# Kernel tuning notes

Hardware: AMD Instinct MI355X
Metric: run time of the kernel (lower is better)

Reference implementation:

```python
import jax, jax.numpy as jnp
import numpy as np

HIDDEN = 1024
JOINTS = 21
IN_DIM = JOINTS * 3  # 63
BATCH = 64
SEQ = 512


def setup_inputs() -> dict:
    key = jax.random.key(0)
    ks = jax.random.split(key, 11)
    s = 0.02
    f32 = jnp.float32
    return {
        "real_seq": jax.random.normal(ks[0], (BATCH, SEQ, IN_DIM), f32),
        # PyTorch nn.GRU params (gates ordered r, z, n)
        "W_ih": jax.random.normal(ks[1], (3 * HIDDEN, IN_DIM), f32) * s,
        "W_hh": jax.random.normal(ks[2], (3 * HIDDEN, HIDDEN), f32) * s,
        "b_ih": jax.random.normal(ks[3], (3 * HIDDEN,), f32) * s,
        "b_hh": jax.random.normal(ks[4], (3 * HIDDEN,), f32) * s,
        # projector MLP (no nonlinearities in the original)
        "W1": jax.random.normal(ks[5], (HIDDEN, HIDDEN), f32) * s,
        "b1": jax.random.normal(ks[6], (HIDDEN,), f32) * s,
        "W2": jax.random.normal(ks[7], (HIDDEN, HIDDEN), f32) * s,
        "b2": jax.random.normal(ks[8], (HIDDEN,), f32) * s,
        "W3": jax.random.normal(ks[9], (IN_DIM, HIDDEN), f32) * s,
        "b3": jax.random.normal(ks[10], (IN_DIM,), f32) * s,
        "condition_length": 5,
        "ground_truth_length": 5,
    }


def _condition_list(seq_len, condition_length, ground_truth_length):
    gt = np.ones((100, ground_truth_length))
    co = np.zeros((100, condition_length))
    return np.concatenate((gt, co), 1).reshape(-1)[:seq_len]


def reference(real_seq, W_ih, W_hh, b_ih, b_hh, W1, b1, W2, b2, W3, b3,
              condition_length, ground_truth_length):
    B, T, D = real_seq.shape
    H = W_hh.shape[1]
    cond = jnp.asarray(_condition_list(T, condition_length, ground_truth_length),
                       dtype=real_seq.dtype)  # [T], static 1/0 teacher-forcing pattern

    h0 = jnp.zeros((B, H), real_seq.dtype)
    o0 = jnp.zeros((B, D), real_seq.dtype)
    xs = (jnp.transpose(real_seq, (1, 0, 2)), cond)  # time-major

    def step(carry, x):
        h, out = carry
        xt, c = x
        inp = jnp.where(c > 0.5, xt, out)  # teacher-forcing switch
        gi = inp @ W_ih.T + b_ih           # [B, 3H]
        gh = h @ W_hh.T + b_hh             # [B, 3H]
        i_r, i_z, i_n = jnp.split(gi, 3, axis=-1)
        h_r, h_z, h_n = jnp.split(gh, 3, axis=-1)
        r = jax.nn.sigmoid(i_r + h_r)
        z = jax.nn.sigmoid(i_z + h_z)
        n = jnp.tanh(i_n + r * h_n)
        h_new = (1.0 - z) * n + z * h
        lin = (h_new @ W1.T + b1) @ W2.T + b2
        out_new = inp + lin @ W3.T + b3    # residual velocities
        return (h_new, out_new), out_new

    _, outs = jax.lax.scan(step, (h0, o0), xs)  # outs: [T, B, D]
    return jnp.transpose(outs, (1, 0, 2)).reshape(B, T, D // 3, 3)
```

## Files before the change

kernel.cpp:

```cpp
#include <hip/hip_runtime.h>
#include <hip/hip_bf16.h>


#define HIDDEN 1024
#define INDIM  63
#define TSEQ   512
#define MB     16
#define NGRP   4
#define NBLK   64
#define HWORDS 512

typedef __attribute__((ext_vector_type(8))) short bfrag8;
typedef __attribute__((ext_vector_type(4))) float ffrag4;
typedef unsigned long long ull;

#define MFMA_B16(a, b, c) __builtin_amdgcn_mfma_f32_16x16x32_bf16((a), (b), (c), 0, 0, 0)

__device__ __forceinline__ short f2bf(float x) {
  __hip_bfloat16 b = __float2bfloat16(x);
  return __builtin_bit_cast(short, b);
}
__device__ __forceinline__ float bf2f(short s) {
  unsigned u = ((unsigned)(unsigned short)s) << 16;
  return __builtin_bit_cast(float, u);
}


__global__ void k_t1(const float* __restrict__ W2, const float* __restrict__ b1,
                     const float* __restrict__ b2, float* __restrict__ t1) {
  const int w = threadIdx.x >> 6, lane = threadIdx.x & 63;
  const int o = blockIdx.x * 4 + w;
  if (o >= HIDDEN) return;
  const float* row = W2 + (size_t)o * HIDDEN;
  float s = 0.f;
  for (int k = lane; k < HIDDEN; k += 64) s += row[k] * b1[k];
  for (int off = 32; off; off >>= 1) s += __shfl_down(s, off, 64);
  if (lane == 0) t1[o] = s + b2[o];
}

__global__ void k_bp(const float* __restrict__ W3, const float* __restrict__ t1,
                     const float* __restrict__ b3, float* __restrict__ bp) {
  const int w = threadIdx.x >> 6, lane = threadIdx.x & 63;
  for (int d = w; d < INDIM; d += 4) {
    const float* row = W3 + (size_t)d * HIDDEN;
    float s = 0.f;
    for (int k = lane; k < HIDDEN; k += 64) s += row[k] * t1[k];
    for (int off = 32; off; off >>= 1) s += __shfl_down(s, off, 64);
    if (lane == 0) bp[d] = s + b3[d];
  }
}

__global__ void k_gemm(const float* __restrict__ A, const float* __restrict__ B,
                       float* __restrict__ C, int M, int N, int K) {
  __shared__ float As[16][17], Bs[16][17];
  const int tx = threadIdx.x, ty = threadIdx.y;
  const int row = blockIdx.y * 16 + ty;
  const int col = blockIdx.x * 16 + tx;
  float acc = 0.f;
  for (int k0 = 0; k0 < K; k0 += 16) {
    As[ty][tx] = (row < M) ? A[(size_t)row * K + k0 + tx] : 0.f;
    Bs[ty][tx] = B[(size_t)(k0 + ty) * N + col];
    __syncthreads();
#pragma unroll
    for (int kk = 0; kk < 16; ++kk) acc += As[ty][kk] * Bs[kk][tx];
    __syncthreads();
  }
  if (row < M && col < N) C[(size_t)row * N + col] = acc;
}


__global__ __launch_bounds__(256, 1) void k_main(
    const float* __restrict__ X,
    const float* __restrict__ W_ih, const float* __restrict__ W_hh,
    const float* __restrict__ b_ih, const float* __restrict__ b_hh,
    const float* __restrict__ WpF, const float* __restrict__ bpF,
    const int* __restrict__ pCL, const int* __restrict__ pGT,
    ull* __restrict__ hb, float* __restrict__ OUT) {
  __shared__ short h_st[MB][HIDDEN + 8];
  __shared__ short inp_bf[MB][88];
  __shared__ float inp_f[MB][68];
  __shared__ float gt_z[MB][16], gt_hn[MB][16];
  __shared__ float gt_ir[MB][16], gt_iz[MB][16], gt_in[MB][16];
  __shared__ short htmp[MB][16];

  const int tid = threadIdx.x;
  const int w = tid >> 6;
  const int lane = tid & 63;
  const int c = lane & 15;
  const int quad = lane >> 4;
  const int g = blockIdx.x >> 6;
  const int j = blockIdx.x & 63;

  const int gtv = pGT[0];
  int period = pCL[0] + gtv;
  if (period < 1) period = 1;

  bfrag8 wB[32];
  bfrag8 wp[32];
  if (w < 3) {
    const float* wr = W_hh + ((size_t)w * HIDDEN + (size_t)j * 16 + c) * HIDDEN;
#pragma unroll
    for (int ks = 0; ks < 32; ++ks) {
      const float* p = wr + ks * 32 + quad * 8;
      bfrag8 f;
#pragma unroll
      for (int e = 0; e < 8; ++e) f[e] = f2bf(p[e]);
      wB[ks] = f;
    }
  } else {
#pragma unroll
    for (int gate = 0; gate < 3; ++gate) {
      const float* wr = W_ih + ((size_t)gate * HIDDEN + (size_t)j * 16 + c) * INDIM;
#pragma unroll
      for (int ks = 0; ks < 2; ++ks) {
        bfrag8 f;
#pragma unroll
        for (int e = 0; e < 8; ++e) {
          int k = ks * 32 + quad * 8 + e;
          f[e] = (k < INDIM) ? f2bf(wr[k]) : (short)0;
        }
        wB[gate * 2 + ks] = f;
      }
    }
  }
  const int dd = 16 * w + c;
  {
    const float* wr = WpF + (size_t)dd * HIDDEN;
#pragma unroll
    for (int ks = 0; ks < 32; ++ks) {
      bfrag8 f;
#pragma unroll
      for (int e = 0; e < 8; ++e)
        f[e] = (dd < INDIM) ? f2bf(wr[ks * 32 + quad * 8 + e]) : (short)0;
      wp[ks] = f;
    }
  }

  float bias_g;
  if (w == 0)      bias_g = b_ih[j * 16 + c] + b_hh[j * 16 + c];
  else if (w == 1) bias_g = b_ih[HIDDEN + j * 16 + c] + b_hh[HIDDEN + j * 16 + c];
  else if (w == 2) bias_g = b_hh[2 * HIDDEN + j * 16 + c];
  else             bias_g = b_ih[2 * HIDDEN + j * 16 + c];
  const float bp_l = (dd < INDIM) ? bpF[dd] : 0.f;

  for (int i = tid; i < MB * (HIDDEN + 8); i += 256) ((short*)h_st)[i] = 0;
  for (int i = tid; i < MB * 88; i += 256) ((short*)inp_bf)[i] = 0;
  for (int i = tid; i < MB * 68; i += 256) ((float*)inp_f)[i] = 0.f;

  ull* hb_g[2] = {hb + (size_t)g * MB * HWORDS,
                  hb + (size_t)(NGRP + g) * MB * HWORDS};

  for (int t = 0; t < TSEQ; ++t) {
    const unsigned tg = (unsigned)(t + 1);
    const bool teach = ((t % period) < gtv);
    if (teach) {
      const int row = tid >> 4, d0 = (tid & 15) * 4;
      const float* xr = X + ((size_t)(g * MB + row) * TSEQ + t) * INDIM;
#pragma unroll
      for (int e = 0; e < 4; ++e) {
        int d = d0 + e;
        float v = (d < INDIM) ? xr[d] : 0.f;
        inp_f[row][d] = v;
        inp_bf[row][d] = f2bf(v);
      }
    }
    __syncthreads();

    ffrag4 ghr;
    float hp[4];
    if (w < 3) {
      ffrag4 acc[4];
#pragma unroll
      for (int e = 0; e < 4; ++e) {
        acc[0][e] = bias_g; acc[1][e] = 0.f; acc[2][e] = 0.f; acc[3][e] = 0.f;
      }
#pragma unroll
      for (int ks = 0; ks < 32; ++ks) {
        const bfrag8 a = *(const bfrag8*)&h_st[c][ks * 32 + quad * 8];
        acc[ks & 3] = MFMA_B16(a, wB[ks], acc[ks & 3]);
      }
      ffrag4 gsum = acc[0] + acc[1] + acc[2] + acc[3];
      if (w == 1) {
#pragma unroll
        for (int i = 0; i < 4; ++i) gt_z[quad * 4 + i][c] = gsum[i];
      } else if (w == 2) {
#pragma unroll
        for (int i = 0; i < 4; ++i) gt_hn[quad * 4 + i][c] = gsum[i];
      } else {
        ghr = gsum;
#pragma unroll
        for (int i = 0; i < 4; ++i) hp[i] = bf2f(h_st[quad * 4 + i][j * 16 + c]);
      }
    } else {
      ffrag4 gir, giz, gin;
#pragma unroll
      for (int e = 0; e < 4; ++e) { gir[e] = 0.f; giz[e] = 0.f; gin[e] = bias_g; }
#pragma unroll
      for (int ks = 0; ks < 2; ++ks) {
        const bfrag8 a = *(const bfrag8*)&inp_bf[c][ks * 32 + quad * 8];
        gir = MFMA_B16(a, wB[0 + ks], gir);
        giz = MFMA_B16(a, wB[2 + ks], giz);
        gin = MFMA_B16(a, wB[4 + ks], gin);
      }
#pragma unroll
      for (int i = 0; i < 4; ++i) {
        gt_ir[quad * 4 + i][c] = gir[i];
        gt_iz[quad * 4 + i][c] = giz[i];
        gt_in[quad * 4 + i][c] = gin[i];
      }
    }
    __syncthreads();

    ull* hw = hb_g[t & 1];
    if (w == 0) {
#pragma unroll
      for (int i = 0; i < 4; ++i) {
        const int row = quad * 4 + i;
        float r = 1.f / (1.f + __expf(-(ghr[i] + gt_ir[row][c])));
        float z = 1.f / (1.f + __expf(-(gt_z[row][c] + gt_iz[row][c])));
        float n = tanhf(gt_in[row][c] + r * gt_hn[row][c]);
        htmp[row][c] = f2bf((1.f - z) * n + z * hp[i]);
      }
      asm volatile("" ::: "memory");
      const int r = lane >> 2, q4 = (lane & 3) * 4;
      unsigned lo0 = (unsigned)(unsigned short)htmp[r][q4 + 0] |
                     ((unsigned)(unsigned short)htmp[r][q4 + 1] << 16);
      unsigned lo1 = (unsigned)(unsigned short)htmp[r][q4 + 2] |
                     ((unsigned)(unsigned short)htmp[r][q4 + 3] << 16);
      ull w0v = ((ull)tg << 32) | lo0;
      ull w1v = ((ull)tg << 32) | lo1;
      ull* dst = hw + (size_t)r * HWORDS + 8 * j + (lane & 3) * 2;
      __hip_atomic_store(dst, w0v, __ATOMIC_RELAXED, __HIP_MEMORY_SCOPE_SYSTEM);
      __hip_atomic_store(dst + 1, w1v, __ATOMIC_RELAXED, __HIP_MEMORY_SCOPE_SYSTEM);
    }

    {
      ull v[32];
#pragma unroll
      for (int s = 0; s < 32; ++s)
        v[s] = __hip_atomic_load(&hw[tid + s * 256], __ATOMIC_RELAXED,
                                 __HIP_MEMORY_SCOPE_SYSTEM);
      bool bad = true;
      while (bad) {
        bad = false;
#pragma unroll
        for (int s = 0; s < 32; ++s) {
          if ((unsigned)(v[s] >> 32) != tg) {
            v[s] = __hip_atomic_load(&hw[tid + s * 256], __ATOMIC_RELAXED,
                                     __HIP_MEMORY_SCOPE_SYSTEM);
            bad = true;
          }
        }
      }
#pragma unroll
      for (int s = 0; s < 32; ++s) {
        const int widx = tid + s * 256;
        *(unsigned*)&h_st[widx >> 9][(widx & 511) * 2] = (unsigned)v[s];
      }
    }
    __syncthreads();

    const bool rep = (t + 1 < TSEQ) && !(((t + 1) % period) < gtv);
    if (rep || j == 0) {
      ffrag4 oa0, oa1;
#pragma unroll
      for (int e = 0; e < 4; ++e) { oa0[e] = bp_l; oa1[e] = 0.f; }
#pragma unroll
      for (int ks = 0; ks < 32; ++ks) {
        const bfrag8 a = *(const bfrag8*)&h_st[c][ks * 32 + quad * 8];
        if (ks & 1) oa1 = MFMA_B16(a, wp[ks], oa1);
        else        oa0 = MFMA_B16(a, wp[ks], oa0);
      }
      ffrag4 o = oa0 + oa1;
#pragma unroll
      for (int i = 0; i < 4; ++i) {
        const int row = quad * 4 + i;
        if (dd < INDIM) {
          float val = o[i] + inp_f[row][dd];
          if (j == 0) OUT[((size_t)(g * MB + row) * TSEQ + t) * INDIM + dd] = val;
          if (rep) { inp_f[row][dd] = val; inp_bf[row][dd] = f2bf(val); }
        } else if (rep) {
          inp_bf[row][dd] = 0;
        }
      }
    }
  }
}


extern "C" void kernel_launch(void* const* d_in, const int* in_sizes, int n_in,
                              void* d_out, int out_size, void* d_ws, size_t ws_size,
                              hipStream_t stream) {
  const float* X    = (const float*)d_in[0];
  const float* W_ih = (const float*)d_in[1];
  const float* W_hh = (const float*)d_in[2];
  const float* b_ih = (const float*)d_in[3];
  const float* b_hh = (const float*)d_in[4];
  const float* W1   = (const float*)d_in[5];
  const float* b1   = (const float*)d_in[6];
  const float* W2   = (const float*)d_in[7];
  const float* b2   = (const float*)d_in[8];
  const float* W3   = (const float*)d_in[9];
  const float* b3   = (const float*)d_in[10];
  const int* pCL    = (const int*)d_in[11];
  const int* pGT    = (const int*)d_in[12];
  float* OUT = (float*)d_out;

  char* ws = (char*)d_ws;
  float* bp = (float*)(ws + 1024);
  float* t1 = (float*)(ws + 2048);
  float* Wp = (float*)(ws + 8192);
  float* T2 = (float*)(ws + 270336);
  ull*   hb = (ull*)(ws + 270336);
  if (ws_size < 795 * 1024) return;

  k_t1<<<256, 256, 0, stream>>>(W2, b1, b2, t1);
  k_gemm<<<dim3(64, 4), dim3(16, 16), 0, stream>>>(W3, W2, T2, INDIM, HIDDEN, HIDDEN);
  k_gemm<<<dim3(64, 4), dim3(16, 16), 0, stream>>>(T2, W1, Wp, INDIM, HIDDEN, HIDDEN);
  k_bp<<<1, 256, 0, stream>>>(W3, t1, b3, bp);
  hipMemsetAsync(hb, 0, 2 * NGRP * MB * HWORDS * sizeof(ull), stream);
  k_main<<<256, 256, 0, stream>>>(X, W_ih, W_hh, b_ih, b_hh, Wp, bp, pCL, pGT, hb, OUT);
}
```

Before: 3.813 ms.

## Fold output projection into GRU input gates and defer output writes off critical path

Precomputes W_ih·Wp (the fused projector composed with the input weights) per block so that, in free-running steps, the input-gate contribution is accumulated as a running sum driven by h via extra MFMAs inside the recurrent matmul, instead of running a separate output projection and then an input-gate matmul after each step. The output projection is moved to four dedicated blocks that compute the previous step's output lagged by one step, and a final pass writes the last step. This is meant to remove the serial projection→input-gate dependency and the extra barrier phase per step. The cost is one extra setup computation, an added __syncthreads per step, doubled MFMAs in the recurrent waves on non-teaching steps, and changed bf16 rounding because the composed weights are quantised.

```diff
diff --git a/kernel.cpp b/kernel.cpp
--- a/kernel.cpp
+++ b/kernel.cpp
@@ -7,7 +7,6 @@
 #define TSEQ   512
 #define MB     16
 #define NGRP   4
-#define NBLK   64
 #define HWORDS 512
 
 typedef __attribute__((ext_vector_type(8))) short bfrag8;
@@ -79,8 +78,8 @@
   __shared__ short h_st[MB][HIDDEN + 8];
   __shared__ short inp_bf[MB][88];
   __shared__ float inp_f[MB][68];
-  __shared__ float gt_z[MB][16], gt_hn[MB][16];
-  __shared__ float gt_ir[MB][16], gt_iz[MB][16], gt_in[MB][16];
+  __shared__ float gt_z[MB][16], gt_un[MB][16], gt_ghn[MB][16];
+  __shared__ float gt_xr[MB][16], gt_xz[MB][16], gt_xn[MB][16];
   __shared__ short htmp[MB][16];
 
   const int tid = threadIdx.x;
@@ -96,7 +95,10 @@
   if (period < 1) period = 1;
 
   bfrag8 wB[32];
-  bfrag8 wp[32];
+  bfrag8 wQ[32];
+  const int dd = 16 * j + c;
+  const bool outw = (w == 3) && (j < 4);
+
   if (w < 3) {
     const float* wr = W_hh + ((size_t)w * HIDDEN + (size_t)j * 16 + c) * HIDDEN;
 #pragma unroll
@@ -122,26 +124,65 @@
         wB[gate * 2 + ks] = f;
       }
     }
-  }
-  const int dd = 16 * w + c;
+    if (outw) {
+      const float* wr = WpF + (size_t)dd * HIDDEN;
+#pragma unroll
+      for (int ks = 0; ks < 32; ++ks) {
+        bfrag8 f;
+#pragma unroll
+        for (int e = 0; e < 8; ++e)
+          f[e] = (dd < INDIM) ? f2bf(wr[ks * 32 + quad * 8 + e]) : (short)0;
+        wQ[ks] = f;
+      }
+    }
+  }
+
+  float bias_g = 0.f, b_ihn_l = 0.f, bp_l = 0.f;
+  if (w == 0) {
+    bias_g = b_ih[j * 16 + c] + b_hh[j * 16 + c];
+    b_ihn_l = b_ih[2 * HIDDEN + j * 16 + c];
+  } else if (w == 1) bias_g = b_ih[HIDDEN + j * 16 + c] + b_hh[HIDDEN + j * 16 + c];
+  else if (w == 2) bias_g = b_hh[2 * HIDDEN + j * 16 + c];
+  else if (outw && dd < INDIM) bp_l = bpF[dd];
+
+  float bq_l = 0.f;
   {
-    const float* wr = WpF + (size_t)dd * HIDDEN;
-#pragma unroll
+    float* WihS = (float*)&h_st[0][0];
+    float* WpS = WihS + 48 * 65;
+    for (int i = tid; i < 48 * 63; i += 256) {
+      int rw = i / 63, d = i - rw * 63;
+      int r = (rw >> 4) * HIDDEN + j * 16 + (rw & 15);
+      WihS[rw * 65 + d] = W_ih[(size_t)r * INDIM + d];
+    }
+    __syncthreads();
+    if (w < 3) {
+      const float* myrow = &WihS[(w * 16 + c) * 65];
+      for (int d = 0; d < INDIM; ++d) bq_l += myrow[d] * bpF[d];
+    }
     for (int ks = 0; ks < 32; ++ks) {
-      bfrag8 f;
-#pragma unroll
-      for (int e = 0; e < 8; ++e)
-        f[e] = (dd < INDIM) ? f2bf(wr[ks * 32 + quad * 8 + e]) : (short)0;
-      wp[ks] = f;
-    }
-  }
-
-  float bias_g;
-  if (w == 0)      bias_g = b_ih[j * 16 + c] + b_hh[j * 16 + c];
-  else if (w == 1) bias_g = b_ih[HIDDEN + j * 16 + c] + b_hh[HIDDEN + j * 16 + c];
-  else if (w == 2) bias_g = b_hh[2 * HIDDEN + j * 16 + c];
-  else             bias_g = b_ih[2 * HIDDEN + j * 16 + c];
-  const float bp_l = (dd < INDIM) ? bpF[dd] : 0.f;
+      __syncthreads();
+      for (int i = tid; i < 63 * 32; i += 256) {
+        int d = i >> 5, kk = i & 31;
+        WpS[d * 33 + kk] = WpF[(size_t)d * HIDDEN + ks * 32 + kk];
+      }
+      __syncthreads();
+      if (w < 3) {
+        const float* myrow = &WihS[(w * 16 + c) * 65];
+        float acc[8] = {0, 0, 0, 0, 0, 0, 0, 0};
+        for (int d = 0; d < INDIM; ++d) {
+          float a = myrow[d];
+          const float* pr = &WpS[d * 33 + quad * 8];
+#pragma unroll
+          for (int e = 0; e < 8; ++e) acc[e] += a * pr[e];
+        }
+        bfrag8 f;
+#pragma unroll
+        for (int e = 0; e < 8; ++e) f[e] = f2bf(acc[e]);
+        wQ[ks] = f;
+      }
+    }
+    __syncthreads();
+  }
 
   for (int i = tid; i < MB * (HIDDEN + 8); i += 256) ((short*)h_st)[i] = 0;
   for (int i = tid; i < MB * 88; i += 256) ((short*)inp_bf)[i] = 0;
@@ -149,6 +190,13 @@
 
   ull* hb_g[2] = {hb + (size_t)g * MB * HWORDS,
                   hb + (size_t)(NGRP + g) * MB * HWORDS};
+
+  ffrag4 up[4];
+#pragma unroll
+  for (int p = 0; p < 4; ++p)
+#pragma unroll
+    for (int e = 0; e < 4; ++e) up[p][e] = 0.f;
+  float inp_reg[4] = {0.f, 0.f, 0.f, 0.f};
 
   for (int t = 0; t < TSEQ; ++t) {
     const unsigned tg = (unsigned)(t + 1);
@@ -174,39 +222,88 @@
       for (int e = 0; e < 4; ++e) {
         acc[0][e] = bias_g; acc[1][e] = 0.f; acc[2][e] = 0.f; acc[3][e] = 0.f;
       }
-#pragma unroll
-      for (int ks = 0; ks < 32; ++ks) {
-        const bfrag8 a = *(const bfrag8*)&h_st[c][ks * 32 + quad * 8];
-        acc[ks & 3] = MFMA_B16(a, wB[ks], acc[ks & 3]);
+      const bool upd = !teach && (t > 0);
+      if (upd) {
+#pragma unroll
+        for (int ks = 0; ks < 32; ++ks) {
+          const bfrag8 a = *(const bfrag8*)&h_st[c][ks * 32 + quad * 8];
+          acc[ks & 3] = MFMA_B16(a, wB[ks], acc[ks & 3]);
+          up[ks & 3] = MFMA_B16(a, wQ[ks], up[ks & 3]);
+        }
+#pragma unroll
+        for (int e = 0; e < 4; ++e) up[0][e] += bq_l;
+      } else {
+#pragma unroll
+        for (int ks = 0; ks < 32; ++ks) {
+          const bfrag8 a = *(const bfrag8*)&h_st[c][ks * 32 + quad * 8];
+          acc[ks & 3] = MFMA_B16(a, wB[ks], acc[ks & 3]);
+        }
       }
       ffrag4 gsum = acc[0] + acc[1] + acc[2] + acc[3];
       if (w == 1) {
 #pragma unroll
-        for (int i = 0; i < 4; ++i) gt_z[quad * 4 + i][c] = gsum[i];
+        for (int i = 0; i < 4; ++i) {
+          float uz = teach ? 0.f : (up[0][i] + up[1][i] + up[2][i] + up[3][i]);
+          gt_z[quad * 4 + i][c] = gsum[i] + uz;
+        }
       } else if (w == 2) {
 #pragma unroll
-        for (int i = 0; i < 4; ++i) gt_hn[quad * 4 + i][c] = gsum[i];
+        for (int i = 0; i < 4; ++i) {
+          gt_ghn[quad * 4 + i][c] = gsum[i];
+          if (!teach)
+            gt_un[quad * 4 + i][c] = up[0][i] + up[1][i] + up[2][i] + up[3][i];
+        }
       } else {
         ghr = gsum;
 #pragma unroll
         for (int i = 0; i < 4; ++i) hp[i] = bf2f(h_st[quad * 4 + i][j * 16 + c]);
       }
     } else {
-      ffrag4 gir, giz, gin;
-#pragma unroll
-      for (int e = 0; e < 4; ++e) { gir[e] = 0.f; giz[e] = 0.f; gin[e] = bias_g; }
-#pragma unroll
-      for (int ks = 0; ks < 2; ++ks) {
-        const bfrag8 a = *(const bfrag8*)&inp_bf[c][ks * 32 + quad * 8];
-        gir = MFMA_B16(a, wB[0 + ks], gir);
-        giz = MFMA_B16(a, wB[2 + ks], giz);
-        gin = MFMA_B16(a, wB[4 + ks], gin);
-      }
-#pragma unroll
-      for (int i = 0; i < 4; ++i) {
-        gt_ir[quad * 4 + i][c] = gir[i];
-        gt_iz[quad * 4 + i][c] = giz[i];
-        gt_in[quad * 4 + i][c] = gin[i];
+      if (outw) {
+        if (t > 0) {
+          ffrag4 oa0, oa1;
+#pragma unroll
+          for (int e = 0; e < 4; ++e) { oa0[e] = bp_l; oa1[e] = 0.f; }
+#pragma unroll
+          for (int ks = 0; ks < 32; ++ks) {
+            const bfrag8 a = *(const bfrag8*)&h_st[c][ks * 32 + quad * 8];
+            if (ks & 1) oa1 = MFMA_B16(a, wQ[ks], oa1);
+            else        oa0 = MFMA_B16(a, wQ[ks], oa0);
+          }
+          ffrag4 o = oa0 + oa1;
+#pragma unroll
+          for (int i = 0; i < 4; ++i) {
+            const int row = quad * 4 + i;
+            if (dd < INDIM) {
+              float val = o[i] + inp_reg[i];
+              OUT[((size_t)(g * MB + row) * TSEQ + (t - 1)) * INDIM + dd] = val;
+              inp_reg[i] = teach ? inp_f[row][dd] : val;
+            }
+          }
+        } else {
+#pragma unroll
+          for (int i = 0; i < 4; ++i)
+            if (dd < INDIM)
+              inp_reg[i] = teach ? inp_f[quad * 4 + i][dd] : 0.f;
+        }
+      }
+      if (teach) {
+        ffrag4 xr, xz, xn;
+#pragma unroll
+        for (int e = 0; e < 4; ++e) { xr[e] = 0.f; xz[e] = 0.f; xn[e] = 0.f; }
+#pragma unroll
+        for (int ks = 0; ks < 2; ++ks) {
+          const bfrag8 a = *(const bfrag8*)&inp_bf[c][ks * 32 + quad * 8];
+          xr = MFMA_B16(a, wB[0 + ks], xr);
+          xz = MFMA_B16(a, wB[2 + ks], xz);
+          xn = MFMA_B16(a, wB[4 + ks], xn);
+        }
+#pragma unroll
+        for (int i = 0; i < 4; ++i) {
+          gt_xr[quad * 4 + i][c] = xr[i];
+          gt_xz[quad * 4 + i][c] = xz[i];
+          gt_xn[quad * 4 + i][c] = xn[i];
+        }
       }
     }
     __syncthreads();
@@ -216,9 +313,13 @@
 #pragma unroll
       for (int i = 0; i < 4; ++i) {
         const int row = quad * 4 + i;
-        float r = 1.f / (1.f + __expf(-(ghr[i] + gt_ir[row][c])));
-        float z = 1.f / (1.f + __expf(-(gt_z[row][c] + gt_iz[row][c])));
-        float n = tanhf(gt_in[row][c] + r * gt_hn[row][c]);
+        float ur = teach ? gt_xr[row][c]
+                         : (up[0][i] + up[1][i] + up[2][i] + up[3][i]);
+        float r = 1.f / (1.f + __expf(-(ghr[i] + ur)));
+        float zt = gt_z[row][c] + (teach ? gt_xz[row][c] : 0.f);
+        float z = 1.f / (1.f + __expf(-zt));
+        float un = teach ? gt_xn[row][c] : gt_un[row][c];
+        float n = tanhf(un + b_ihn_l + r * gt_ghn[row][c]);
         htmp[row][c] = f2bf((1.f - z) * n + z * hp[i]);
       }
       asm volatile("" ::: "memory");
@@ -233,6 +334,16 @@
       __hip_atomic_store(dst, w0v, __ATOMIC_RELAXED, __HIP_MEMORY_SCOPE_SYSTEM);
       __hip_atomic_store(dst + 1, w1v, __ATOMIC_RELAXED, __HIP_MEMORY_SCOPE_SYSTEM);
     }
+    if (teach && w < 3) {
+#pragma unroll
+      for (int i = 0; i < 4; ++i) {
+        float v = (w == 0) ? gt_xr[quad * 4 + i][c]
+                : (w == 1) ? gt_xz[quad * 4 + i][c]
+                           : gt_xn[quad * 4 + i][c];
+        up[0][i] = v; up[1][i] = 0.f; up[2][i] = 0.f; up[3][i] = 0.f;
+      }
+    }
+    __syncthreads();
 
     {
       ull v[32];
@@ -259,30 +370,25 @@
       }
     }
     __syncthreads();
-
-    const bool rep = (t + 1 < TSEQ) && !(((t + 1) % period) < gtv);
-    if (rep || j == 0) {
-      ffrag4 oa0, oa1;
-#pragma unroll
-      for (int e = 0; e < 4; ++e) { oa0[e] = bp_l; oa1[e] = 0.f; }
-#pragma unroll
-      for (int ks = 0; ks < 32; ++ks) {
-        const bfrag8 a = *(const bfrag8*)&h_st[c][ks * 32 + quad * 8];
-        if (ks & 1) oa1 = MFMA_B16(a, wp[ks], oa1);
-        else        oa0 = MFMA_B16(a, wp[ks], oa0);
-      }
-      ffrag4 o = oa0 + oa1;
-#pragma unroll
-      for (int i = 0; i < 4; ++i) {
-        const int row = quad * 4 + i;
-        if (dd < INDIM) {
-          float val = o[i] + inp_f[row][dd];
-          if (j == 0) OUT[((size_t)(g * MB + row) * TSEQ + t) * INDIM + dd] = val;
-          if (rep) { inp_f[row][dd] = val; inp_bf[row][dd] = f2bf(val); }
-        } else if (rep) {
-          inp_bf[row][dd] = 0;
-        }
-      }
+  }
+
+  if (outw) {
+    ffrag4 oa0, oa1;
+#pragma unroll
+    for (int e = 0; e < 4; ++e) { oa0[e] = bp_l; oa1[e] = 0.f; }
+#pragma unroll
+    for (int ks = 0; ks < 32; ++ks) {
+      const bfrag8 a = *(const bfrag8*)&h_st[c][ks * 32 + quad * 8];
+      if (ks & 1) oa1 = MFMA_B16(a, wQ[ks], oa1);
+      else        oa0 = MFMA_B16(a, wQ[ks], oa0);
+    }
+    ffrag4 o = oa0 + oa1;
+#pragma unroll
+    for (int i = 0; i < 4; ++i) {
+      const int row = quad * 4 + i;
+      if (dd < INDIM)
+        OUT[((size_t)(g * MB + row) * TSEQ + (TSEQ - 1)) * INDIM + dd] =
+            o[i] + inp_reg[i];
     }
   }
 }
```

Measured after the change: 5.380 ms. 41.1% more time.

## Process two batch groups per block to overlap cross-block exchange latency

Applied to the files above, without the earlier changes.

Each persistent block now handles two batch groups (A and B) instead of one, halving the grid to 128 blocks. Group B's recurrent GEMM and publication are interleaved so that group A's global hidden-state exchange wait overlaps with B's compute, and B's wait overlaps with A's projector work. The aim is to hide the inter-block spin-wait latency per timestep. The cost is doubled shared memory, extra syncs per step, and twice the serial compute per block on half as many CUs.

```diff
diff --git a/kernel.cpp b/kernel.cpp
--- a/kernel.cpp
+++ b/kernel.cpp
@@ -7,7 +7,6 @@
 #define TSEQ   512
 #define MB     16
 #define NGRP   4
-#define NBLK   64
 #define HWORDS 512
 
 typedef __attribute__((ext_vector_type(8))) short bfrag8;
@@ -76,20 +75,20 @@
     const float* __restrict__ WpF, const float* __restrict__ bpF,
     const int* __restrict__ pCL, const int* __restrict__ pGT,
     ull* __restrict__ hb, float* __restrict__ OUT) {
-  __shared__ short h_st[MB][HIDDEN + 8];
-  __shared__ short inp_bf[MB][88];
-  __shared__ float inp_f[MB][68];
-  __shared__ float gt_z[MB][16], gt_hn[MB][16];
-  __shared__ float gt_ir[MB][16], gt_iz[MB][16], gt_in[MB][16];
-  __shared__ short htmp[MB][16];
+  __shared__ short h_stA[MB][HIDDEN + 8], h_stB[MB][HIDDEN + 8];
+  __shared__ short inpbA[MB][88], inpbB[MB][88];
+  __shared__ float inpfA[MB][68], inpfB[MB][68];
+  __shared__ float tA[6][MB][17], tB[6][MB][17];
+  __shared__ short htA[MB][16], htB[MB][16];
 
   const int tid = threadIdx.x;
   const int w = tid >> 6;
   const int lane = tid & 63;
   const int c = lane & 15;
   const int quad = lane >> 4;
-  const int g = blockIdx.x >> 6;
+  const int p = blockIdx.x >> 6;
   const int j = blockIdx.x & 63;
+  const int grpA = 2 * p, grpB = 2 * p + 1;
 
   const int gtv = pGT[0];
   int period = pCL[0] + gtv;
@@ -101,10 +100,10 @@
     const float* wr = W_hh + ((size_t)w * HIDDEN + (size_t)j * 16 + c) * HIDDEN;
 #pragma unroll
     for (int ks = 0; ks < 32; ++ks) {
-      const float* p = wr + ks * 32 + quad * 8;
+      const float* pw = wr + ks * 32 + quad * 8;
       bfrag8 f;
 #pragma unroll
-      for (int e = 0; e < 8; ++e) f[e] = f2bf(p[e]);
+      for (int e = 0; e < 8; ++e) f[e] = f2bf(pw[e]);
       wB[ks] = f;
     }
   } else {
@@ -143,31 +142,41 @@
   else             bias_g = b_ih[2 * HIDDEN + j * 16 + c];
   const float bp_l = (dd < INDIM) ? bpF[dd] : 0.f;
 
-  for (int i = tid; i < MB * (HIDDEN + 8); i += 256) ((short*)h_st)[i] = 0;
-  for (int i = tid; i < MB * 88; i += 256) ((short*)inp_bf)[i] = 0;
-  for (int i = tid; i < MB * 68; i += 256) ((float*)inp_f)[i] = 0.f;
-
-  ull* hb_g[2] = {hb + (size_t)g * MB * HWORDS,
-                  hb + (size_t)(NGRP + g) * MB * HWORDS};
+  for (int i = tid; i < MB * (HIDDEN + 8); i += 256) {
+    ((short*)h_stA)[i] = 0; ((short*)h_stB)[i] = 0;
+  }
+  for (int i = tid; i < MB * 88; i += 256) {
+    ((short*)inpbA)[i] = 0; ((short*)inpbB)[i] = 0;
+  }
+  for (int i = tid; i < MB * 68; i += 256) {
+    ((float*)inpfA)[i] = 0.f; ((float*)inpfB)[i] = 0.f;
+  }
+
+  ull* hbA[2] = {hb + (size_t)grpA * MB * HWORDS,
+                 hb + (size_t)(NGRP + grpA) * MB * HWORDS};
+  ull* hbB[2] = {hb + (size_t)grpB * MB * HWORDS,
+                 hb + (size_t)(NGRP + grpB) * MB * HWORDS};
 
   for (int t = 0; t < TSEQ; ++t) {
     const unsigned tg = (unsigned)(t + 1);
     const bool teach = ((t % period) < gtv);
+    const bool rep = (t + 1 < TSEQ) && !(((t + 1) % period) < gtv);
+
     if (teach) {
       const int row = tid >> 4, d0 = (tid & 15) * 4;
-      const float* xr = X + ((size_t)(g * MB + row) * TSEQ + t) * INDIM;
+      const float* xa = X + ((size_t)(grpA * MB + row) * TSEQ + t) * INDIM;
+      const float* xb = X + ((size_t)(grpB * MB + row) * TSEQ + t) * INDIM;
 #pragma unroll
       for (int e = 0; e < 4; ++e) {
         int d = d0 + e;
-        float v = (d < INDIM) ? xr[d] : 0.f;
-        inp_f[row][d] = v;
-        inp_bf[row][d] = f2bf(v);
-      }
-    }
-    __syncthreads();
-
-    ffrag4 ghr;
-    float hp[4];
+        float va = (d < INDIM) ? xa[d] : 0.f;
+        float vb = (d < INDIM) ? xb[d] : 0.f;
+        inpfA[row][d] = va; inpbA[row][d] = f2bf(va);
+        inpfB[row][d] = vb; inpbB[row][d] = f2bf(vb);
+      }
+    }
+    __syncthreads();
+
     if (w < 3) {
       ffrag4 acc[4];
 #pragma unroll
@@ -176,69 +185,119 @@
       }
 #pragma unroll
       for (int ks = 0; ks < 32; ++ks) {
-        const bfrag8 a = *(const bfrag8*)&h_st[c][ks * 32 + quad * 8];
+        const bfrag8 a = *(const bfrag8*)&h_stA[c][ks * 32 + quad * 8];
         acc[ks & 3] = MFMA_B16(a, wB[ks], acc[ks & 3]);
       }
-      ffrag4 gsum = acc[0] + acc[1] + acc[2] + acc[3];
-      if (w == 1) {
-#pragma unroll
-        for (int i = 0; i < 4; ++i) gt_z[quad * 4 + i][c] = gsum[i];
-      } else if (w == 2) {
-#pragma unroll
-        for (int i = 0; i < 4; ++i) gt_hn[quad * 4 + i][c] = gsum[i];
-      } else {
-        ghr = gsum;
-#pragma unroll
-        for (int i = 0; i < 4; ++i) hp[i] = bf2f(h_st[quad * 4 + i][j * 16 + c]);
-      }
+      ffrag4 gs = acc[0] + acc[1] + acc[2] + acc[3];
+#pragma unroll
+      for (int i = 0; i < 4; ++i) tA[w][quad * 4 + i][c] = gs[i];
     } else {
       ffrag4 gir, giz, gin;
 #pragma unroll
       for (int e = 0; e < 4; ++e) { gir[e] = 0.f; giz[e] = 0.f; gin[e] = bias_g; }
 #pragma unroll
       for (int ks = 0; ks < 2; ++ks) {
-        const bfrag8 a = *(const bfrag8*)&inp_bf[c][ks * 32 + quad * 8];
+        const bfrag8 a = *(const bfrag8*)&inpbA[c][ks * 32 + quad * 8];
         gir = MFMA_B16(a, wB[0 + ks], gir);
         giz = MFMA_B16(a, wB[2 + ks], giz);
         gin = MFMA_B16(a, wB[4 + ks], gin);
       }
 #pragma unroll
       for (int i = 0; i < 4; ++i) {
-        gt_ir[quad * 4 + i][c] = gir[i];
-        gt_iz[quad * 4 + i][c] = giz[i];
-        gt_in[quad * 4 + i][c] = gin[i];
-      }
-    }
-    __syncthreads();
-
-    ull* hw = hb_g[t & 1];
+        tA[3][quad * 4 + i][c] = gir[i];
+        tA[4][quad * 4 + i][c] = giz[i];
+        tA[5][quad * 4 + i][c] = gin[i];
+      }
+    }
+    __syncthreads();
+
+    ull* hwA = hbA[t & 1];
     if (w == 0) {
 #pragma unroll
       for (int i = 0; i < 4; ++i) {
         const int row = quad * 4 + i;
-        float r = 1.f / (1.f + __expf(-(ghr[i] + gt_ir[row][c])));
-        float z = 1.f / (1.f + __expf(-(gt_z[row][c] + gt_iz[row][c])));
-        float n = tanhf(gt_in[row][c] + r * gt_hn[row][c]);
-        htmp[row][c] = f2bf((1.f - z) * n + z * hp[i]);
+        float r = 1.f / (1.f + __expf(-(tA[0][row][c] + tA[3][row][c])));
+        float z = 1.f / (1.f + __expf(-(tA[1][row][c] + tA[4][row][c])));
+        float n = tanhf(tA[5][row][c] + r * tA[2][row][c]);
+        float hp = bf2f(h_stA[row][j * 16 + c]);
+        htA[row][c] = f2bf((1.f - z) * n + z * hp);
       }
       asm volatile("" ::: "memory");
-      const int r = lane >> 2, q4 = (lane & 3) * 4;
-      unsigned lo0 = (unsigned)(unsigned short)htmp[r][q4 + 0] |
-                     ((unsigned)(unsigned short)htmp[r][q4 + 1] << 16);
-      unsigned lo1 = (unsigned)(unsigned short)htmp[r][q4 + 2] |
-                     ((unsigned)(unsigned short)htmp[r][q4 + 3] << 16);
-      ull w0v = ((ull)tg << 32) | lo0;
-      ull w1v = ((ull)tg << 32) | lo1;
-      ull* dst = hw + (size_t)r * HWORDS + 8 * j + (lane & 3) * 2;
-      __hip_atomic_store(dst, w0v, __ATOMIC_RELAXED, __HIP_MEMORY_SCOPE_SYSTEM);
-      __hip_atomic_store(dst + 1, w1v, __ATOMIC_RELAXED, __HIP_MEMORY_SCOPE_SYSTEM);
+      const int r2 = lane >> 2, q4 = (lane & 3) * 4;
+      unsigned lo0 = (unsigned)(unsigned short)htA[r2][q4 + 0] |
+                     ((unsigned)(unsigned short)htA[r2][q4 + 1] << 16);
+      unsigned lo1 = (unsigned)(unsigned short)htA[r2][q4 + 2] |
+                     ((unsigned)(unsigned short)htA[r2][q4 + 3] << 16);
+      ull* dst = hwA + (size_t)r2 * HWORDS + 8 * j + (lane & 3) * 2;
+      __hip_atomic_store(dst, ((ull)tg << 32) | lo0,
+                         __ATOMIC_RELAXED, __HIP_MEMORY_SCOPE_SYSTEM);
+      __hip_atomic_store(dst + 1, ((ull)tg << 32) | lo1,
+                         __ATOMIC_RELAXED, __HIP_MEMORY_SCOPE_SYSTEM);
+    }
+
+    if (w < 3) {
+      ffrag4 acc[4];
+#pragma unroll
+      for (int e = 0; e < 4; ++e) {
+        acc[0][e] = bias_g; acc[1][e] = 0.f; acc[2][e] = 0.f; acc[3][e] = 0.f;
+      }
+#pragma unroll
+      for (int ks = 0; ks < 32; ++ks) {
+        const bfrag8 a = *(const bfrag8*)&h_stB[c][ks * 32 + quad * 8];
+        acc[ks & 3] = MFMA_B16(a, wB[ks], acc[ks & 3]);
+      }
+      ffrag4 gs = acc[0] + acc[1] + acc[2] + acc[3];
+#pragma unroll
+      for (int i = 0; i < 4; ++i) tB[w][quad * 4 + i][c] = gs[i];
+    } else {
+      ffrag4 gir, giz, gin;
+#pragma unroll
+      for (int e = 0; e < 4; ++e) { gir[e] = 0.f; giz[e] = 0.f; gin[e] = bias_g; }
+#pragma unroll
+      for (int ks = 0; ks < 2; ++ks) {
+        const bfrag8 a = *(const bfrag8*)&inpbB[c][ks * 32 + quad * 8];
+        gir = MFMA_B16(a, wB[0 + ks], gir);
+        giz = MFMA_B16(a, wB[2 + ks], giz);
+        gin = MFMA_B16(a, wB[4 + ks], gin);
+      }
+#pragma unroll
+      for (int i = 0; i < 4; ++i) {
+        tB[3][quad * 4 + i][c] = gir[i];
+        tB[4][quad * 4 + i][c] = giz[i];
+        tB[5][quad * 4 + i][c] = gin[i];
+      }
+    }
+    __syncthreads();
+
+    ull* hwB = hbB[t & 1];
+    if (w == 1) {
+#pragma unroll
+      for (int i = 0; i < 4; ++i) {
+        const int row = quad * 4 + i;
+        float r = 1.f / (1.f + __expf(-(tB[0][row][c] + tB[3][row][c])));
+        float z = 1.f / (1.f + __expf(-(tB[1][row][c] + tB[4][row][c])));
+        float n = tanhf(tB[5][row][c] + r * tB[2][row][c]);
+        float hp = bf2f(h_stB[row][j * 16 + c]);
+        htB[row][c] = f2bf((1.f - z) * n + z * hp);
+      }
+      asm volatile("" ::: "memory");
+      const int r2 = lane >> 2, q4 = (lane & 3) * 4;
+      unsigned lo0 = (unsigned)(unsigned short)htB[r2][q4 + 0] |
+                     ((unsigned)(unsigned short)htB[r2][q4 + 1] << 16);
+      unsigned lo1 = (unsigned)(unsigned short)htB[r2][q4 + 2] |
+                     ((unsigned)(unsigned short)htB[r2][q4 + 3] << 16);
+      ull* dst = hwB + (size_t)r2 * HWORDS + 8 * j + (lane & 3) * 2;
+      __hip_atomic_store(dst, ((ull)tg << 32) | lo0,
+                         __ATOMIC_RELAXED, __HIP_MEMORY_SCOPE_SYSTEM);
+      __hip_atomic_store(dst + 1, ((ull)tg << 32) | lo1,
+                         __ATOMIC_RELAXED, __HIP_MEMORY_SCOPE_SYSTEM);
     }
 
     {
       ull v[32];
 #pragma unroll
       for (int s = 0; s < 32; ++s)
-        v[s] = __hip_atomic_load(&hw[tid + s * 256], __ATOMIC_RELAXED,
+        v[s] = __hip_atomic_load(&hwA[tid + s * 256], __ATOMIC_RELAXED,
                                  __HIP_MEMORY_SCOPE_SYSTEM);
       bool bad = true;
       while (bad) {
@@ -246,7 +305,7 @@
 #pragma unroll
         for (int s = 0; s < 32; ++s) {
           if ((unsigned)(v[s] >> 32) != tg) {
-            v[s] = __hip_atomic_load(&hw[tid + s * 256], __ATOMIC_RELAXED,
+            v[s] = __hip_atomic_load(&hwA[tid + s * 256], __ATOMIC_RELAXED,
                                      __HIP_MEMORY_SCOPE_SYSTEM);
             bad = true;
           }
@@ -255,19 +314,18 @@
 #pragma unroll
       for (int s = 0; s < 32; ++s) {
         const int widx = tid + s * 256;
-        *(unsigned*)&h_st[widx >> 9][(widx & 511) * 2] = (unsigned)v[s];
-      }
-    }
-    __syncthreads();
-
-    const bool rep = (t + 1 < TSEQ) && !(((t + 1) % period) < gtv);
+        *(unsigned*)&h_stA[widx >> 9][(widx & 511) * 2] = (unsigned)v[s];
+      }
+    }
+    __syncthreads();
+
     if (rep || j == 0) {
       ffrag4 oa0, oa1;
 #pragma unroll
       for (int e = 0; e < 4; ++e) { oa0[e] = bp_l; oa1[e] = 0.f; }
 #pragma unroll
       for (int ks = 0; ks < 32; ++ks) {
-        const bfrag8 a = *(const bfrag8*)&h_st[c][ks * 32 + quad * 8];
+        const bfrag8 a = *(const bfrag8*)&h_stA[c][ks * 32 + quad * 8];
         if (ks & 1) oa1 = MFMA_B16(a, wp[ks], oa1);
         else        oa0 = MFMA_B16(a, wp[ks], oa0);
       }
@@ -276,14 +334,65 @@
       for (int i = 0; i < 4; ++i) {
         const int row = quad * 4 + i;
         if (dd < INDIM) {
-          float val = o[i] + inp_f[row][dd];
-          if (j == 0) OUT[((size_t)(g * MB + row) * TSEQ + t) * INDIM + dd] = val;
-          if (rep) { inp_f[row][dd] = val; inp_bf[row][dd] = f2bf(val); }
+          float val = o[i] + inpfA[row][dd];
+          if (j == 0) OUT[((size_t)(grpA * MB + row) * TSEQ + t) * INDIM + dd] = val;
+          if (rep) { inpfA[row][dd] = val; inpbA[row][dd] = f2bf(val); }
         } else if (rep) {
-          inp_bf[row][dd] = 0;
+          inpbA[row][dd] = 0;
         }
       }
     }
+
+    {
+      ull v[32];
+#pragma unroll
+      for (int s = 0; s < 32; ++s)
+        v[s] = __hip_atomic_load(&hwB[tid + s * 256], __ATOMIC_RELAXED,
+                                 __HIP_MEMORY_SCOPE_SYSTEM);
+      bool bad = true;
+      while (bad) {
+        bad = false;
+#pragma unroll
+        for (int s = 0; s < 32; ++s) {
+          if ((unsigned)(v[s] >> 32) != tg) {
+            v[s] = __hip_atomic_load(&hwB[tid + s * 256], __ATOMIC_RELAXED,
+                                     __HIP_MEMORY_SCOPE_SYSTEM);
+            bad = true;
+          }
+        }
+      }
+#pragma unroll
+      for (int s = 0; s < 32; ++s) {
+        const int widx = tid + s * 256;
+        *(unsigned*)&h_stB[widx >> 9][(widx & 511) * 2] = (unsigned)v[s];
+      }
+    }
+    __syncthreads();
+
+    if (rep || j == 0) {
+      ffrag4 oa0, oa1;
+#pragma unroll
+      for (int e = 0; e < 4; ++e) { oa0[e] = bp_l; oa1[e] = 0.f; }
+#pragma unroll
+      for (int ks = 0; ks < 32; ++ks) {
+        const bfrag8 a = *(const bfrag8*)&h_stB[c][ks * 32 + quad * 8];
+        if (ks & 1) oa1 = MFMA_B16(a, wp[ks], oa1);
+        else        oa0 = MFMA_B16(a, wp[ks], oa0);
+      }
+      ffrag4 o = oa0 + oa1;
+#pragma unroll
+      for (int i = 0; i < 4; ++i) {
+        const int row = quad * 4 + i;
+        if (dd < INDIM) {
+          float val = o[i] + inpfB[row][dd];
+          if (j == 0) OUT[((size_t)(grpB * MB + row) * TSEQ + t) * INDIM + dd] = val;
+          if (rep) { inpfB[row][dd] = val; inpbB[row][dd] = f2bf(val); }
+        } else if (rep) {
+          inpbB[row][dd] = 0;
+        }
+      }
+    }
+    __syncthreads();
   }
 }
 
@@ -319,5 +428,5 @@
   k_gemm<<<dim3(64, 4), dim3(16, 16), 0, stream>>>(T2, W1, Wp, INDIM, HIDDEN, HIDDEN);
   k_bp<<<1, 256, 0, stream>>>(W3, t1, b3, bp);
   hipMemsetAsync(hb, 0, 2 * NGRP * MB * HWORDS * sizeof(ull), stream);
-  k_main<<<256, 256, 0, stream>>>(X, W_ih, W_hh, b_ih, b_hh, Wp, bp, pCL, pGT, hb, OUT);
-}
+  k_main<<<128, 256, 0, stream>>>(X, W_ih, W_hh, b_ih, b_hh, Wp, bp, pCL, pGT, hb, OUT);
+}
```

After: 5.924 ms. +55.3%, slower.
